# Kernel tuning notes

Measured on AMD Instinct MI355X. Metric: run time of the kernel, lower is better.

## Reference

```python
import jax, jax.numpy as jnp
import numpy as np

N_NODES = 100000
N_EDGES = 1600000
N_GRAPHS = 128
CONV = [64, 64, 64]
HID = [256, 128, 2]
GFT = 64
EPS = 1e-5
NEG_SLOPE = 0.01


def leaky_relu(x):
    return jnp.where(x >= 0, x, NEG_SLOPE * x)


def setup_inputs() -> dict:
    key = jax.random.key(0)
    ks = jax.random.split(key, 32)
    inp = {}
    inp['x'] = jax.random.normal(ks[0], (N_NODES, CONV[0]), dtype=jnp.float32)
    inp['edge_index'] = jax.random.randint(ks[1], (2, N_EDGES), 0, N_NODES, dtype=jnp.int64)
    inp['graph_features'] = jax.random.normal(ks[2], (N_GRAPHS, GFT), dtype=jnp.float32)
    inp['batch'] = jnp.sort(jax.random.randint(ks[3], (N_NODES,), 0, N_GRAPHS, dtype=jnp.int64))
    # SAGEConv params per layer: W_l (aggregated branch, with bias), W_r (root branch), BN gamma/beta
    ki = 4
    for li in range(len(CONV) - 1):
        fin, fout = CONV[li], CONV[li + 1]
        s = 1.0 / np.sqrt(fin)
        inp[f'Wl{li}'] = jax.random.uniform(ks[ki], (fin, fout), minval=-s, maxval=s); ki += 1
        inp[f'bl{li}'] = jax.random.uniform(ks[ki], (fout,), minval=-s, maxval=s); ki += 1
        inp[f'Wr{li}'] = jax.random.uniform(ks[ki], (fin, fout), minval=-s, maxval=s); ki += 1
        inp[f'g{li}'] = jnp.ones((fout,), jnp.float32)
        inp[f'b{li}'] = jnp.zeros((fout,), jnp.float32)
    # MLP: Linear(128->256), LeakyReLU, Linear(256->128), LeakyReLU, Linear(128->2)
    dims = [CONV[-1] + GFT] + HID
    for li in range(len(HID)):
        fin, fout = dims[li], dims[li + 1]
        s = 1.0 / np.sqrt(fin)
        inp[f'Wm{li}'] = jax.random.uniform(ks[ki], (fin, fout), minval=-s, maxval=s); ki += 1
        inp[f'bm{li}'] = jax.random.uniform(ks[ki], (fout,), minval=-s, maxval=s); ki += 1
    return inp


def _sage_block(x, src, dst, Wl, bl, Wr, gamma, beta):
    # PyG SAGEConv (aggr='mean'): out = lin_l(mean_{j in N(i)} x_j) + lin_r(x_i)
    msgs = x[src]                                               # [E, Fin] gather
    agg = jax.ops.segment_sum(msgs, dst, num_segments=N_NODES)  # [N, Fin] scatter-add
    deg = jax.ops.segment_sum(jnp.ones((src.shape[0],), x.dtype), dst, num_segments=N_NODES)
    agg = agg / jnp.maximum(deg, 1.0)[:, None]
    h = agg @ Wl + bl + x @ Wr
    h = leaky_relu(h)
    # BatchNorm1d (training mode: batch stats over nodes, biased variance)
    mu = h.mean(axis=0)
    var = h.var(axis=0)
    return (h - mu) * jax.lax.rsqrt(var + EPS) * gamma + beta


def reference(x, edge_index, graph_features, batch,
              Wl0, bl0, Wr0, g0, b0, Wl1, bl1, Wr1, g1, b1,
              Wm0, bm0, Wm1, bm1, Wm2, bm2):
    src, dst = edge_index[0], edge_index[1]
    h = _sage_block(x, src, dst, Wl0, bl0, Wr0, g0, b0)
    h = _sage_block(h, src, dst, Wl1, bl1, Wr1, g1, b1)
    # scatter_mean graph pooling
    pooled = jax.ops.segment_sum(h, batch, num_segments=N_GRAPHS)
    cnt = jax.ops.segment_sum(jnp.ones((h.shape[0],), h.dtype), batch, num_segments=N_GRAPHS)
    pooled = pooled / jnp.maximum(cnt, 1.0)[:, None]
    z = jnp.concatenate([pooled, graph_features], axis=1)       # [G, 128]
    z = leaky_relu(z @ Wm0 + bm0)
    z = leaky_relu(z @ Wm1 + bm1)
    return z @ Wm2 + bm2
```

## Files before the change

kernel.cpp:

```cpp
#include <hip/hip_runtime.h>

#define N_NODES 100000
#define N_EDGES 1600000
#define N_GRAPHS 128
#define FDIM 64
#define EPSV 1e-5f
#define NEG 0.01f

#define NB 782
#define PART_BLOCKS 391
#define CVT_BLOCKS 1563
#define NTILES 6250
#define TPB 2
#define GEMM_BLOCKS 3125
#define BN_SLOTS 128

typedef short bf16x8 __attribute__((ext_vector_type(8)));
typedef float f32x4  __attribute__((ext_vector_type(4)));

__device__ __forceinline__ float leaky(float x){ return x >= 0.f ? x : NEG*x; }

__device__ __forceinline__ unsigned short f2bf(float x){
    unsigned u = __float_as_uint(x);
    return (unsigned short)((u + 0x7fffu + ((u >> 16) & 1u)) >> 16);
}
__device__ __forceinline__ float bf2f(unsigned short b){
    return __uint_as_float(((unsigned)b) << 16);
}

__global__ __launch_bounds__(256) void k_prep(const float* __restrict__ x,
                                              unsigned short* __restrict__ o,
                                              const int* __restrict__ dst,
                                              int* __restrict__ bhist,
                                              float* __restrict__ bnpart){
    __shared__ int lh[NB];
    int b = blockIdx.x, t = threadIdx.x;
    if (b < CVT_BLOCKS){
        int base = b*1024 + t;
        #pragma unroll
        for (int k2 = 0; k2 < 4; ++k2){
            int i = base + k2*256;
            if (i < (N_NODES*FDIM)/4){
                float4 v = ((const float4*)x)[i];
                ushort4 r;
                r.x = f2bf(v.x); r.y = f2bf(v.y); r.z = f2bf(v.z); r.w = f2bf(v.w);
                ((ushort4*)o)[i] = r;
            }
        }
        if (b < 64) bnpart[(b << 8) + t] = 0.f;
    } else {
        for (int i = t; i < NB; i += 256) lh[i] = 0;
        __syncthreads();
        int base = (b - CVT_BLOCKS) * 4096;
        #pragma unroll
        for (int k = 0; k < 16; ++k){
            int e = base + k*256 + t;
            if (e < N_EDGES) atomicAdd(&lh[dst[e] >> 7], 1);
        }
        __syncthreads();
        for (int i = t; i < NB; i += 256) if (lh[i]) atomicAdd(&bhist[i], lh[i]);
    }
}

__global__ __launch_bounds__(256) void k_bscan(const int* __restrict__ bhist,
                                               int* __restrict__ boff, int* __restrict__ cur){
    __shared__ int lds[256];
    int t = threadIdx.x;
    int base = t*4;
    int v0 = (base+0 < NB) ? bhist[base+0] : 0;
    int v1 = (base+1 < NB) ? bhist[base+1] : 0;
    int v2 = (base+2 < NB) ? bhist[base+2] : 0;
    int v3 = (base+3 < NB) ? bhist[base+3] : 0;
    lds[t] = v0+v1+v2+v3; __syncthreads();
    for (int off = 1; off < 256; off <<= 1){
        int add = (t >= off) ? lds[t-off] : 0; __syncthreads();
        lds[t] += add; __syncthreads();
    }
    int excl = (t > 0) ? lds[t-1] : 0;
    int p0 = excl, p1 = excl+v0, p2 = excl+v0+v1, p3 = excl+v0+v1+v2;
    if (base+0 < NB){ boff[base+0] = p0; cur[base+0] = p0; }
    if (base+1 < NB){ boff[base+1] = p1; cur[base+1] = p1; }
    if (base+2 < NB){ boff[base+2] = p2; cur[base+2] = p2; }
    if (base+3 < NB){ boff[base+3] = p3; cur[base+3] = p3; }
    if (t == 0) boff[NB] = N_EDGES;
}

__global__ __launch_bounds__(256) void k_part(const int* __restrict__ src, const int* __restrict__ dst,
                                              int* __restrict__ cur, int* __restrict__ packed){
    __shared__ int lh[NB];
    __shared__ int lc[NB];
    int t = threadIdx.x;
    for (int i = t; i < NB; i += 256) lh[i] = 0;
    __syncthreads();
    int base = blockIdx.x * 4096;
    int d[16];
    #pragma unroll
    for (int k = 0; k < 16; ++k){
        int e = base + k*256 + t;
        d[k] = (e < N_EDGES) ? dst[e] : -1;
        if (d[k] >= 0) atomicAdd(&lh[d[k] >> 7], 1);
    }
    __syncthreads();
    for (int i = t; i < NB; i += 256) lc[i] = atomicAdd(&cur[i], lh[i]);
    __syncthreads();
    #pragma unroll
    for (int k = 0; k < 16; ++k){
        int e = base + k*256 + t;
        if (e < N_EDGES){
            int b = d[k] >> 7;
            int p = atomicAdd(&lc[b], 1);
            packed[p] = (src[e] << 7) | (d[k] & 127);
        }
    }
}

__global__ __launch_bounds__(256) void k_sort(const int* __restrict__ packed,
                                              const int* __restrict__ boff,
                                              int* __restrict__ rs, int* __restrict__ colb){
    __shared__ int hist[128];
    __shared__ int curs[128];
    int b = blockIdx.x, t = threadIdx.x;
    int e0 = boff[b], e1 = boff[b+1];
    if (t < 128) hist[t] = 0;
    __syncthreads();
    for (int e = e0 + t; e < e1; e += 256)
        atomicAdd(&hist[packed[e] & 127], 1);
    __syncthreads();
    int cnt = (t < 128) ? hist[t] : 0;
    __syncthreads();
    for (int off = 1; off < 128; off <<= 1){
        int add = (t < 128 && t >= off) ? hist[t-off] : 0;
        __syncthreads();
        if (t < 128) hist[t] += add;
        __syncthreads();
    }
    int nbase = b << 7;
    int nloc = min(128, N_NODES - nbase);
    if (t < nloc){
        int excl = hist[t] - cnt;
        rs[nbase + t] = e0 + excl;
        curs[t] = excl;
    }
    __syncthreads();
    for (int e = e0 + t; e < e1; e += 256){
        int v = packed[e];
        int p = atomicAdd(&curs[v & 127], 1);
        colb[e0 + p] = v & 0xFFFFFF80;
    }
    if (b == 0 && t == 0) rs[N_NODES] = N_EDGES;
}

__global__ __launch_bounds__(256) void k_agg(
    const unsigned short* __restrict__ xin, const int* __restrict__ rs,
    const int* __restrict__ colb, unsigned short* __restrict__ agg)
{
    int t = threadIdx.x;
    int lane = t & 63;
    int sub = lane >> 4;
    int q   = lane & 15;
    const char* xb = (const char*)xin + (q << 3);
    int wid = (blockIdx.x << 2) + (t >> 6);
    const int nw = gridDim.x << 2;
    for (int n = wid; n < N_NODES; n += nw){
        int e0 = __builtin_amdgcn_readfirstlane(rs[n]);
        int e1 = __builtin_amdgcn_readfirstlane(rs[n+1]);
        float ax=0.f, ay=0.f, az=0.f, aw=0.f;
        for (int e = e0; e < e1; e += 16){
            int i0 = e + sub, i1 = e + 4 + sub, i2 = e + 8 + sub, i3 = e + 12 + sub;
            if (i0 < e1){
                uint2 u = *(const uint2*)(xb + colb[i0]);
                ax += __uint_as_float(u.x << 16); ay += __uint_as_float(u.x & 0xffff0000u);
                az += __uint_as_float(u.y << 16); aw += __uint_as_float(u.y & 0xffff0000u);
            }
            if (i1 < e1){
                uint2 u = *(const uint2*)(xb + colb[i1]);
                ax += __uint_as_float(u.x << 16); ay += __uint_as_float(u.x & 0xffff0000u);
                az += __uint_as_float(u.y << 16); aw += __uint_as_float(u.y & 0xffff0000u);
            }
            if (i2 < e1){
                uint2 u = *(const uint2*)(xb + colb[i2]);
                ax += __uint_as_float(u.x << 16); ay += __uint_as_float(u.x & 0xffff0000u);
                az += __uint_as_float(u.y << 16); aw += __uint_as_float(u.y & 0xffff0000u);
            }
            if (i3 < e1){
                uint2 u = *(const uint2*)(xb + colb[i3]);
                ax += __uint_as_float(u.x << 16); ay += __uint_as_float(u.x & 0xffff0000u);
                az += __uint_as_float(u.y << 16); aw += __uint_as_float(u.y & 0xffff0000u);
            }
        }
        ax += __shfl_xor(ax, 16, 64); ay += __shfl_xor(ay, 16, 64);
        az += __shfl_xor(az, 16, 64); aw += __shfl_xor(aw, 16, 64);
        ax += __shfl_xor(ax, 32, 64); ay += __shfl_xor(ay, 32, 64);
        az += __shfl_xor(az, 32, 64); aw += __shfl_xor(aw, 32, 64);
        if (sub == 0){
            float rd = 1.f / fmaxf((float)(e1 - e0), 1.f);
            ushort4 o;
            o.x = f2bf(ax*rd); o.y = f2bf(ay*rd);
            o.z = f2bf(az*rd); o.w = f2bf(aw*rd);
            *(ushort4*)((char*)agg + (((size_t)n) << 7) + (q << 3)) = o;
        }
    }
}

template<bool AFF>
__global__ __launch_bounds__(256) void k_gemm(
    const unsigned short* __restrict__ agg,
    const unsigned short* __restrict__ xin,
    unsigned short* __restrict__ hout,
    const int* __restrict__ rs, const int* __restrict__ batch,
    const float* __restrict__ Wl, const float* __restrict__ Wr,
    const float* __restrict__ scale,
    const float* __restrict__ bbias, const float* __restrict__ bdelta,
    float* __restrict__ bnpart, float* __restrict__ S)
{
    __shared__ float sS[8*64];
    int t = threadIdx.x;
    int lane = t & 63;
    int jt = t >> 6;
    int g = lane >> 4, r = lane & 15;
    int j = (jt << 4) + r;

    bf16x8 wlh[2], wll[2], wrh[2], wrl[2];
    #pragma unroll
    for (int ks = 0; ks < 2; ++ks){
        #pragma unroll
        for (int i = 0; i < 8; ++i){
            int k = (ks << 5) + (g << 3) + i;
            float s = AFF ? scale[k] : 1.f;
            float wv = Wl[(k << 6) + j] * s;
            unsigned u = __float_as_uint(wv);
            wlh[ks][i] = (short)(u >> 16);
            float lf = wv - __uint_as_float(u & 0xffff0000u);
            wll[ks][i] = (short)(__float_as_uint(lf) >> 16);
            wv = Wr[(k << 6) + j] * s;
            u = __float_as_uint(wv);
            wrh[ks][i] = (short)(u >> 16);
            lf = wv - __uint_as_float(u & 0xffff0000u);
            wrl[ks][i] = (short)(__float_as_uint(lf) >> 16);
        }
    }

    float bb = bbias[j];
    float bd = AFF ? bdelta[j] : 0.f;

    int gbase = 0, span = 0;
    if (AFF){
        for (int i = t; i < 512; i += 256) sS[i] = 0.f;
        int nfirst = blockIdx.x * (TPB*16);
        int nlast  = min(nfirst + TPB*16 - 1, N_NODES - 1);
        gbase = batch[nfirst];
        span  = batch[nlast] - gbase + 1;
        __syncthreads();
    }

    float bs = 0.f, bq = 0.f;
    int c0 = blockIdx.x * TPB;

    auto LOADT = [&](int tile, bf16x8* A, bf16x8* X, int4& R, int& R5, int4& B){
        size_t rowoff = (((size_t)((tile << 4) + r)) << 6) + (g << 3);
        const bf16x8* pa = (const bf16x8*)(agg + rowoff);
        const bf16x8* px = (const bf16x8*)(xin + rowoff);
        A[0] = pa[0]; A[1] = pa[4];
        X[0] = px[0]; X[1] = px[4];
        if (AFF){
            int nb = (tile << 4) + (g << 2);
            R  = *(const int4*)(rs + nb);
            R5 = rs[nb + 4];
            B  = *(const int4*)(batch + nb);
        }
    };

    auto POOL = [&](int gr, float hv){
        int lg = gr - gbase;
        if (lg < 8) atomicAdd(&sS[(lg << 6) + j], hv);
        else        atomicAdd(&S[(gr << 6) + j], hv);
    };

    auto COMPUTE = [&](int tile, const bf16x8* A, const bf16x8* X,
                       const int4& R, int R5, const int4& B){
        f32x4 accA = {0.f, 0.f, 0.f, 0.f};
        f32x4 accX = {0.f, 0.f, 0.f, 0.f};
        accA = __builtin_amdgcn_mfma_f32_16x16x32_bf16(A[0], wlh[0], accA, 0, 0, 0);
        accA = __builtin_amdgcn_mfma_f32_16x16x32_bf16(A[0], wll[0], accA, 0, 0, 0);
        accA = __builtin_amdgcn_mfma_f32_16x16x32_bf16(A[1], wlh[1], accA, 0, 0, 0);
        accA = __builtin_amdgcn_mfma_f32_16x16x32_bf16(A[1], wll[1], accA, 0, 0, 0);
        accX = __builtin_amdgcn_mfma_f32_16x16x32_bf16(X[0], wrh[0], accX, 0, 0, 0);
        accX = __builtin_amdgcn_mfma_f32_16x16x32_bf16(X[0], wrl[0], accX, 0, 0, 0);
        accX = __builtin_amdgcn_mfma_f32_16x16x32_bf16(X[1], wrh[1], accX, 0, 0, 0);
        accX = __builtin_amdgcn_mfma_f32_16x16x32_bf16(X[1], wrl[1], accX, 0, 0, 0);

        int nb = (tile << 4) + (g << 2);
        if (AFF){
            float hv;
            hv = accA[0] + accX[0] + bb + ((R.y - R.x) > 0 ? bd : 0.f);
            hv = leaky(hv); bs += hv; bq += hv*hv; POOL(B.x, hv);
            hv = accA[1] + accX[1] + bb + ((R.z - R.y) > 0 ? bd : 0.f);
            hv = leaky(hv); bs += hv; bq += hv*hv; POOL(B.y, hv);
            hv = accA[2] + accX[2] + bb + ((R.w - R.z) > 0 ? bd : 0.f);
            hv = leaky(hv); bs += hv; bq += hv*hv; POOL(B.z, hv);
            hv = accA[3] + accX[3] + bb + ((R5 - R.w) > 0 ? bd : 0.f);
            hv = leaky(hv); bs += hv; bq += hv*hv; POOL(B.w, hv);
        } else {
            #pragma unroll
            for (int q = 0; q < 4; ++q){
                float hv = leaky(accA[q] + accX[q] + bb);
                unsigned short h16 = f2bf(hv);
                float hr = bf2f(h16);
                hout[((size_t)(nb + q) << 6) + j] = h16;
                bs += hr; bq += hr*hr;
            }
        }
    };

    bf16x8 Aa[2], Xa[2], Ab[2], Xb[2];
    int4 Ra = {0,0,0,0}, Rb = {0,0,0,0}, Ba = {0,0,0,0}, Bb = {0,0,0,0};
    int R5a = 0, R5b = 0;

    LOADT(c0 + 0, Aa, Xa, Ra, R5a, Ba);
    LOADT(c0 + 1, Ab, Xb, Rb, R5b, Bb);
    COMPUTE(c0 + 0, Aa, Xa, Ra, R5a, Ba);
    COMPUTE(c0 + 1, Ab, Xb, Rb, R5b, Bb);

    bs += __shfl_xor(bs, 16, 64); bs += __shfl_xor(bs, 32, 64);
    bq += __shfl_xor(bq, 16, 64); bq += __shfl_xor(bq, 32, 64);
    if (lane < 16){
        float* bp = bnpart + ((blockIdx.x & (BN_SLOTS-1)) * 128);
        atomicAdd(&bp[(jt << 4) + lane], bs);
        atomicAdd(&bp[64 + (jt << 4) + lane], bq);
    }

    if (AFF){
        __syncthreads();
        int sp = min(span, 8);
        for (int i = t; i < (sp << 6); i += 256){
            float v = sS[i];
            if (v != 0.f) atomicAdd(&S[((gbase + (i >> 6)) << 6) + (i & 63)], v);
        }
    }
}

template<bool FOLD>
__global__ __launch_bounds__(256) void k_bnfin(
    float* __restrict__ bnpart,
    const float* __restrict__ gamma, const float* __restrict__ beta,
    const float* __restrict__ Wl_nx, const float* __restrict__ Wr_nx,
    const float* __restrict__ bl_nx,
    float* __restrict__ scale, float* __restrict__ shift,
    float* __restrict__ bbias, float* __restrict__ bdelta,
    float* __restrict__ Szero)
{
    __shared__ float ssh[64];
    int t = threadIdx.x;
    if (t < 64){
        int j = t;
        float s = 0.f, q = 0.f;
        #pragma unroll 8
        for (int i = 0; i < BN_SLOTS; ++i){
            s += bnpart[i*128 + j];
            q += bnpart[i*128 + 64 + j];
        }
        float mu  = s * (1.0f/N_NODES);
        float var = q * (1.0f/N_NODES) - mu*mu;
        float sc  = gamma[j] * rsqrtf(var + EPSV);
        float sh  = beta[j] - mu*sc;
        scale[j] = sc; shift[j] = sh;
        ssh[j] = sh;
    }
    __syncthreads();
    if (FOLD){
        if (t < 64){
            int j = t;
            float bbv = bl_nx[j], bdv = 0.f;
            #pragma unroll 8
            for (int k = 0; k < 64; ++k){
                bbv += ssh[k] * Wr_nx[(k << 6) + j];
                bdv += ssh[k] * Wl_nx[(k << 6) + j];
            }
            bbias[j] = bbv; bdelta[j] = bdv;
        }
        __syncthreads();
        for (int i = t; i < BN_SLOTS*128; i += 256) bnpart[i] = 0.f;
        for (int i = t; i < N_GRAPHS*FDIM; i += 256) Szero[i] = 0.f;
    }
}

__global__ __launch_bounds__(256) void k_mlp(
    const float* __restrict__ S, const int* __restrict__ batch,
    const float* __restrict__ scale, const float* __restrict__ shift,
    const float* __restrict__ gf,
    const float* __restrict__ Wm0, const float* __restrict__ bm0,
    const float* __restrict__ Wm1, const float* __restrict__ bm1,
    const float* __restrict__ Wm2, const float* __restrict__ bm2,
    float* __restrict__ out)
{
    __shared__ int seg[2];
    __shared__ float z[128];
    __shared__ float h1[256];
    __shared__ float h2[128];
    int g = blockIdx.x, t = threadIdx.x;
    if (t < 2){
        int target = g + t;
        int lo = 0, hi = N_NODES;
        while (lo < hi){ int mid = (lo+hi)>>1; if (batch[mid] < target) lo = mid+1; else hi = mid; }
        seg[t] = lo;
    }
    __syncthreads();
    float cnt = (float)(seg[1] - seg[0]);
    if (t < 64)
        z[t] = (scale[t]*S[(g<<6)+t] + cnt*shift[t]) / fmaxf(cnt, 1.f);
    else if (t < 128)
        z[t] = gf[g*64 + (t-64)];
    __syncthreads();
    float acc = bm0[t];
    #pragma unroll 8
    for (int k = 0; k < 128; ++k) acc += z[k]*Wm0[k*256 + t];
    h1[t] = leaky(acc);
    __syncthreads();
    if (t < 128){
        float a = bm1[t];
        #pragma unroll 8
        for (int k = 0; k < 256; ++k) a += h1[k]*Wm1[k*128 + t];
        h2[t] = leaky(a);
    }
    __syncthreads();
    if (t < 2){
        float a = bm2[t];
        for (int k = 0; k < 128; ++k) a += h2[k]*Wm2[k*2 + t];
        out[g*2 + t] = a;
    }
}

extern "C" void kernel_launch(void* const* d_in, const int* in_sizes, int n_in,
                              void* d_out, int out_size, void* d_ws, size_t ws_size,
                              hipStream_t stream) {
    const float* x     = (const float*)d_in[0];
    const int*   ei    = (const int*)d_in[1];
    const float* gf    = (const float*)d_in[2];
    const int*   batch = (const int*)d_in[3];
    const float* Wl0 = (const float*)d_in[4];
    const float* bl0 = (const float*)d_in[5];
    const float* Wr0 = (const float*)d_in[6];
    const float* g0  = (const float*)d_in[7];
    const float* b0  = (const float*)d_in[8];
    const float* Wl1 = (const float*)d_in[9];
    const float* bl1 = (const float*)d_in[10];
    const float* Wr1 = (const float*)d_in[11];
    const float* g1  = (const float*)d_in[12];
    const float* b1  = (const float*)d_in[13];
    const float* Wm0 = (const float*)d_in[14];
    const float* bm0 = (const float*)d_in[15];
    const float* Wm1 = (const float*)d_in[16];
    const float* bm1 = (const float*)d_in[17];
    const float* Wm2 = (const float*)d_in[18];
    const float* bm2 = (const float*)d_in[19];

    int*   bhist  = (int*)d_ws;
    int*   boff   = bhist + NB;
    int*   cur    = boff + NB + 1;
    int*   packed = (int*)d_ws + 2348;
    int*   rs     = packed + N_EDGES;
    int*   colb   = rs + 100004;
    unsigned short* xbf   = (unsigned short*)(colb + N_EDGES);
    unsigned short* h1bf  = xbf + (size_t)N_NODES*FDIM;
    unsigned short* aggbf = h1bf + (size_t)N_NODES*FDIM;
    float* bnpart = (float*)(aggbf + (size_t)N_NODES*FDIM);
    float* S      = bnpart + BN_SLOTS*128;
    float* scale0 = S + N_GRAPHS*FDIM;
    float* shift0 = scale0 + 64;
    float* scale1 = scale0 + 128;
    float* shift1 = scale0 + 192;
    float* bbias  = scale0 + 256;
    float* bdelta = scale0 + 320;

    const int* srcp = ei;
    const int* dstp = ei + N_EDGES;

    hipMemsetAsync(bhist, 0, NB*sizeof(int), stream);
    k_prep<<<CVT_BLOCKS + PART_BLOCKS, 256, 0, stream>>>(x, xbf, dstp, bhist, bnpart);
    k_bscan<<<1, 256, 0, stream>>>(bhist, boff, cur);
    k_part<<<PART_BLOCKS, 256, 0, stream>>>(srcp, dstp, cur, packed);
    k_sort<<<NB, 256, 0, stream>>>(packed, boff, rs, colb);

    k_agg<<<2048, 256, 0, stream>>>(xbf, rs, colb, aggbf);
    k_gemm<false><<<GEMM_BLOCKS, 256, 0, stream>>>(
        aggbf, xbf, h1bf, rs, batch,
        Wl0, Wr0, nullptr, bl0, nullptr, bnpart, nullptr);
    k_bnfin<true><<<1, 256, 0, stream>>>(bnpart, g0, b0, Wl1, Wr1, bl1,
                                         scale0, shift0, bbias, bdelta, S);

    k_agg<<<2048, 256, 0, stream>>>(h1bf, rs, colb, aggbf);
    k_gemm<true><<<GEMM_BLOCKS, 256, 0, stream>>>(
        aggbf, h1bf, nullptr, rs, batch,
        Wl1, Wr1, scale0, bbias, bdelta, bnpart, S);
    k_bnfin<false><<<1, 256, 0, stream>>>(bnpart, g1, b1, nullptr, nullptr, nullptr,
                                          scale1, shift1, nullptr, nullptr, nullptr);

    k_mlp<<<N_GRAPHS, 256, 0, stream>>>(S, batch, scale1, shift1, gf,
                                        Wm0, bm0, Wm1, bm1, Wm2, bm2, (float*)d_out);
}
```

Before: 283.7 us.

## Process two nodes per wavefront in aggregation and move buffer zeroing to prep

The aggregation kernel now has each wavefront handle two adjacent nodes at once, interleaving their index loads and feature gathers so more memory requests are in flight per wave. Each node now gets 8 edges per iteration instead of 16. Separately, the BN partial-sum buffers are split into two copies and zeroed, together with the pooling accumulator, in the prep kernel, so the single-block bnfin kernel no longer has to clear them serially. The risk is more divergence when the two nodes have very different degrees, and higher register pressure from the doubled accumulators.

Measured after the change: 283.6 us. About the same (-0.0%).

```diff
diff --git a/kernel.cpp b/kernel.cpp
--- a/kernel.cpp
+++ b/kernel.cpp
@@ -32,7 +32,7 @@
                                               unsigned short* __restrict__ o,
                                               const int* __restrict__ dst,
                                               int* __restrict__ bhist,
-                                              float* __restrict__ bnpart){
+                                              float* __restrict__ zbase){
     __shared__ int lh[NB];
     int b = blockIdx.x, t = threadIdx.x;
     if (b < CVT_BLOCKS){
@@ -47,7 +47,7 @@
                 ((ushort4*)o)[i] = r;
             }
         }
-        if (b < 64) bnpart[(b << 8) + t] = 0.f;
+        if (b < 160) zbase[(b << 8) + t] = 0.f;
     } else {
         for (int i = t; i < NB; i += 256) lh[i] = 0;
         __syncthreads();
@@ -161,43 +161,65 @@
     const char* xb = (const char*)xin + (q << 3);
     int wid = (blockIdx.x << 2) + (t >> 6);
     const int nw = gridDim.x << 2;
-    for (int n = wid; n < N_NODES; n += nw){
-        int e0 = __builtin_amdgcn_readfirstlane(rs[n]);
-        int e1 = __builtin_amdgcn_readfirstlane(rs[n+1]);
-        float ax=0.f, ay=0.f, az=0.f, aw=0.f;
-        for (int e = e0; e < e1; e += 16){
-            int i0 = e + sub, i1 = e + 4 + sub, i2 = e + 8 + sub, i3 = e + 12 + sub;
-            if (i0 < e1){
-                uint2 u = *(const uint2*)(xb + colb[i0]);
-                ax += __uint_as_float(u.x << 16); ay += __uint_as_float(u.x & 0xffff0000u);
-                az += __uint_as_float(u.y << 16); aw += __uint_as_float(u.y & 0xffff0000u);
+    for (int n0 = wid << 1; n0 < N_NODES; n0 += (nw << 1)){
+        int e0a = __builtin_amdgcn_readfirstlane(rs[n0]);
+        int e1a = __builtin_amdgcn_readfirstlane(rs[n0+1]);
+        int e1b = __builtin_amdgcn_readfirstlane(rs[n0+2]);
+        int ea = e0a, eb = e1a;
+        float axA=0.f, ayA=0.f, azA=0.f, awA=0.f;
+        float axB=0.f, ayB=0.f, azB=0.f, awB=0.f;
+        while (ea < e1a || eb < e1b){
+            int ia0 = ea + sub, ia1 = ea + 4 + sub;
+            int ib0 = eb + sub, ib1 = eb + 4 + sub;
+            bool va0 = ia0 < e1a, va1 = ia1 < e1a;
+            bool vb0 = ib0 < e1b, vb1 = ib1 < e1b;
+            int ca0, ca1, cb0, cb1;
+            if (va0) ca0 = colb[ia0];
+            if (va1) ca1 = colb[ia1];
+            if (vb0) cb0 = colb[ib0];
+            if (vb1) cb1 = colb[ib1];
+            if (va0){
+                uint2 u = *(const uint2*)(xb + ca0);
+                axA += __uint_as_float(u.x << 16); ayA += __uint_as_float(u.x & 0xffff0000u);
+                azA += __uint_as_float(u.y << 16); awA += __uint_as_float(u.y & 0xffff0000u);
             }
-            if (i1 < e1){
-                uint2 u = *(const uint2*)(xb + colb[i1]);
-                ax += __uint_as_float(u.x << 16); ay += __uint_as_float(u.x & 0xffff0000u);
-                az += __uint_as_float(u.y << 16); aw += __uint_as_float(u.y & 0xffff0000u);
+            if (vb0){
+                uint2 u = *(const uint2*)(xb + cb0);
+                axB += __uint_as_float(u.x << 16); ayB += __uint_as_float(u.x & 0xffff0000u);
+                azB += __uint_as_float(u.y << 16); awB += __uint_as_float(u.y & 0xffff0000u);
             }
-            if (i2 < e1){
-                uint2 u = *(const uint2*)(xb + colb[i2]);
-                ax += __uint_as_float(u.x << 16); ay += __uint_as_float(u.x & 0xffff0000u);
-                az += __uint_as_float(u.y << 16); aw += __uint_as_float(u.y & 0xffff0000u);
+            if (va1){
+                uint2 u = *(const uint2*)(xb + ca1);
+                axA += __uint_as_float(u.x << 16); ayA += __uint_as_float(u.x & 0xffff0000u);
+                azA += __uint_as_float(u.y << 16); awA += __uint_as_float(u.y & 0xffff0000u);
             }
-            if (i3 < e1){
-                uint2 u = *(const uint2*)(xb + colb[i3]);
-                ax += __uint_as_float(u.x << 16); ay += __uint_as_float(u.x & 0xffff0000u);
-                az += __uint_as_float(u.y << 16); aw += __uint_as_float(u.y & 0xffff0000u);
+            if (vb1){
+                uint2 u = *(const uint2*)(xb + cb1);
+                axB += __uint_as_float(u.x << 16); ayB += __uint_as_float(u.x & 0xffff0000u);
+                azB += __uint_as_float(u.y << 16); awB += __uint_as_float(u.y & 0xffff0000u);
             }
-        }
-        ax += __shfl_xor(ax, 16, 64); ay += __shfl_xor(ay, 16, 64);
-        az += __shfl_xor(az, 16, 64); aw += __shfl_xor(aw, 16, 64);
-        ax += __shfl_xor(ax, 32, 64); ay += __shfl_xor(ay, 32, 64);
-        az += __shfl_xor(az, 32, 64); aw += __shfl_xor(aw, 32, 64);
+            ea += 8; eb += 8;
+        }
+        axA += __shfl_xor(axA, 16, 64); ayA += __shfl_xor(ayA, 16, 64);
+        azA += __shfl_xor(azA, 16, 64); awA += __shfl_xor(awA, 16, 64);
+        axB += __shfl_xor(axB, 16, 64); ayB += __shfl_xor(ayB, 16, 64);
+        azB += __shfl_xor(azB, 16, 64); awB += __shfl_xor(awB, 16, 64);
+        axA += __shfl_xor(axA, 32, 64); ayA += __shfl_xor(ayA, 32, 64);
+        azA += __shfl_xor(azA, 32, 64); awA += __shfl_xor(awA, 32, 64);
+        axB += __shfl_xor(axB, 32, 64); ayB += __shfl_xor(ayB, 32, 64);
+        azB += __shfl_xor(azB, 32, 64); awB += __shfl_xor(awB, 32, 64);
         if (sub == 0){
-            float rd = 1.f / fmaxf((float)(e1 - e0), 1.f);
+            float rd = 1.f / fmaxf((float)(e1a - e0a), 1.f);
             ushort4 o;
-            o.x = f2bf(ax*rd); o.y = f2bf(ay*rd);
-            o.z = f2bf(az*rd); o.w = f2bf(aw*rd);
-            *(ushort4*)((char*)agg + (((size_t)n) << 7) + (q << 3)) = o;
+            o.x = f2bf(axA*rd); o.y = f2bf(ayA*rd);
+            o.z = f2bf(azA*rd); o.w = f2bf(awA*rd);
+            *(ushort4*)((char*)agg + (((size_t)n0) << 7) + (q << 3)) = o;
+        } else if (sub == 1){
+            float rd = 1.f / fmaxf((float)(e1b - e1a), 1.f);
+            ushort4 o;
+            o.x = f2bf(axB*rd); o.y = f2bf(ayB*rd);
+            o.z = f2bf(azB*rd); o.w = f2bf(awB*rd);
+            *(ushort4*)((char*)agg + (((size_t)(n0+1)) << 7) + (q << 3)) = o;
         }
     }
 }
@@ -302,11 +324,11 @@
             hv = leaky(hv); bs += hv; bq += hv*hv; POOL(B.w, hv);
         } else {
             #pragma unroll
-            for (int q = 0; q < 4; ++q){
-                float hv = leaky(accA[q] + accX[q] + bb);
+            for (int q2 = 0; q2 < 4; ++q2){
+                float hv = leaky(accA[q2] + accX[q2] + bb);
                 unsigned short h16 = f2bf(hv);
                 float hr = bf2f(h16);
-                hout[((size_t)(nb + q) << 6) + j] = h16;
+                hout[((size_t)(nb + q2) << 6) + j] = h16;
                 bs += hr; bq += hr*hr;
             }
         }
@@ -341,13 +363,12 @@
 
 template<bool FOLD>
 __global__ __launch_bounds__(256) void k_bnfin(
-    float* __restrict__ bnpart,
+    const float* __restrict__ bnpart,
     const float* __restrict__ gamma, const float* __restrict__ beta,
     const float* __restrict__ Wl_nx, const float* __restrict__ Wr_nx,
     const float* __restrict__ bl_nx,
     float* __restrict__ scale, float* __restrict__ shift,
-    float* __restrict__ bbias, float* __restrict__ bdelta,
-    float* __restrict__ Szero)
+    float* __restrict__ bbias, float* __restrict__ bdelta)
 {
     __shared__ float ssh[64];
     int t = threadIdx.x;
@@ -367,20 +388,15 @@
         ssh[j] = sh;
     }
     __syncthreads();
-    if (FOLD){
-        if (t < 64){
-            int j = t;
-            float bbv = bl_nx[j], bdv = 0.f;
-            #pragma unroll 8
-            for (int k = 0; k < 64; ++k){
-                bbv += ssh[k] * Wr_nx[(k << 6) + j];
-                bdv += ssh[k] * Wl_nx[(k << 6) + j];
-            }
-            bbias[j] = bbv; bdelta[j] = bdv;
-        }
-        __syncthreads();
-        for (int i = t; i < BN_SLOTS*128; i += 256) bnpart[i] = 0.f;
-        for (int i = t; i < N_GRAPHS*FDIM; i += 256) Szero[i] = 0.f;
+    if (FOLD && t < 64){
+        int j = t;
+        float bbv = bl_nx[j], bdv = 0.f;
+        #pragma unroll 8
+        for (int k = 0; k < 64; ++k){
+            bbv += ssh[k] * Wr_nx[(k << 6) + j];
+            bdv += ssh[k] * Wl_nx[(k << 6) + j];
+        }
+        bbias[j] = bbv; bdelta[j] = bdv;
     }
 }
 
@@ -463,20 +479,21 @@
     unsigned short* xbf   = (unsigned short*)(colb + N_EDGES);
     unsigned short* h1bf  = xbf + (size_t)N_NODES*FDIM;
     unsigned short* aggbf = h1bf + (size_t)N_NODES*FDIM;
-    float* bnpart = (float*)(aggbf + (size_t)N_NODES*FDIM);
-    float* S      = bnpart + BN_SLOTS*128;
-    float* scale0 = S + N_GRAPHS*FDIM;
-    float* shift0 = scale0 + 64;
-    float* scale1 = scale0 + 128;
-    float* shift1 = scale0 + 192;
-    float* bbias  = scale0 + 256;
-    float* bdelta = scale0 + 320;
+    float* bnpartA = (float*)(aggbf + (size_t)N_NODES*FDIM);
+    float* bnpartB = bnpartA + BN_SLOTS*128;
+    float* S       = bnpartB + BN_SLOTS*128;
+    float* scale0  = S + N_GRAPHS*FDIM;
+    float* shift0  = scale0 + 64;
+    float* scale1  = scale0 + 128;
+    float* shift1  = scale0 + 192;
+    float* bbias   = scale0 + 256;
+    float* bdelta  = scale0 + 320;
 
     const int* srcp = ei;
     const int* dstp = ei + N_EDGES;
 
     hipMemsetAsync(bhist, 0, NB*sizeof(int), stream);
-    k_prep<<<CVT_BLOCKS + PART_BLOCKS, 256, 0, stream>>>(x, xbf, dstp, bhist, bnpart);
+    k_prep<<<CVT_BLOCKS + PART_BLOCKS, 256, 0, stream>>>(x, xbf, dstp, bhist, bnpartA);
     k_bscan<<<1, 256, 0, stream>>>(bhist, boff, cur);
     k_part<<<PART_BLOCKS, 256, 0, stream>>>(srcp, dstp, cur, packed);
     k_sort<<<NB, 256, 0, stream>>>(packed, boff, rs, colb);
@@ -484,16 +501,16 @@
     k_agg<<<2048, 256, 0, stream>>>(xbf, rs, colb, aggbf);
     k_gemm<false><<<GEMM_BLOCKS, 256, 0, stream>>>(
         aggbf, xbf, h1bf, rs, batch,
-        Wl0, Wr0, nullptr, bl0, nullptr, bnpart, nullptr);
-    k_bnfin<true><<<1, 256, 0, stream>>>(bnpart, g0, b0, Wl1, Wr1, bl1,
-                                         scale0, shift0, bbias, bdelta, S);
+        Wl0, Wr0, nullptr, bl0, nullptr, bnpartA, nullptr);
+    k_bnfin<true><<<1, 256, 0, stream>>>(bnpartA, g0, b0, Wl1, Wr1, bl1,
+                                         scale0, shift0, bbias, bdelta);
 
     k_agg<<<2048, 256, 0, stream>>>(h1bf, rs, colb, aggbf);
     k_gemm<true><<<GEMM_BLOCKS, 256, 0, stream>>>(
         aggbf, h1bf, nullptr, rs, batch,
-        Wl1, Wr1, scale0, bbias, bdelta, bnpart, S);
-    k_bnfin<false><<<1, 256, 0, stream>>>(bnpart, g1, b1, nullptr, nullptr, nullptr,
-                                          scale1, shift1, nullptr, nullptr, nullptr);
+        Wl1, Wr1, scale0, bbias, bdelta, bnpartB, S);
+    k_bnfin<false><<<1, 256, 0, stream>>>(bnpartB, g1, b1, nullptr, nullptr, nullptr,
+                                          scale1, shift1, nullptr, nullptr);
 
     k_mlp<<<N_GRAPHS, 256, 0, stream>>>(S, batch, scale1, shift1, gf,
                                         Wm0, bm0, Wm1, bm1, Wm2, bm2, (float*)d_out);
```
